# Kernel optimization log

Measured on AMD Instinct MI355X. Metric: run time of the kernel, lower is better.

Reference implementation:

```python
import jax, jax.numpy as jnp
import numpy as np

IN_F = 256
OUT_F = 512
DEG = 3
BATCH = 2048


def setup_inputs() -> dict:
    key = jax.random.key(0)
    k_x, k_p, k_q, k_w = jax.random.split(key, 4)
    x = jax.random.normal(k_x, (BATCH, IN_F), dtype=jnp.float32)
    P_coef = jax.random.normal(k_p, (OUT_F, IN_F, DEG + 1), dtype=jnp.float32) * 0.1
    Q_coef = jax.random.normal(k_q, (OUT_F, IN_F, DEG), dtype=jnp.float32) * 0.1
    # reset_parameters(): constant term of P zeroed, constant of Q set to 1
    P_coef = P_coef.at[:, :, 0].set(0.0)
    Q_coef = Q_coef.at[:, :, 0].set(1.0)
    # xavier_uniform for base_weight
    limit = float(np.sqrt(6.0 / (IN_F + OUT_F)))
    base_weight = jax.random.uniform(k_w, (OUT_F, IN_F), dtype=jnp.float32,
                                     minval=-limit, maxval=limit)
    base_bias = jnp.zeros((OUT_F,), dtype=jnp.float32)
    return {"x": x, "P_coef": P_coef, "Q_coef": Q_coef,
            "base_weight": base_weight, "base_bias": base_bias}


def reference(x, P_coef, Q_coef, base_weight, base_bias):
    # x: (B, I). Powers x^0..x^DEG -> (B, I, DEG+1)
    exps = jnp.arange(DEG + 1, dtype=x.dtype)
    x_powers = x[..., None] ** exps  # (B, I, P)
    # P[b,i,o] = sum_p P_coef[o,i,p] * x[b,i]^p
    P = jnp.einsum('oip,bip->bio', P_coef, x_powers)
    # Q uses powers x^1..x^DEG
    Q = 1.0 + jnp.einsum('oip,bip->bio', Q_coef, x_powers[:, :, 1:])
    rational = P / (Q + 1e-6)          # (B, I, O)
    rational_output = rational.sum(axis=1)  # (B, O)
    base_output = x @ base_weight.T + base_bias  # (B, O)
    return base_output + rational_output
```

## Files before the change

### kernel.cpp

```cpp
#include <hip/hip_runtime.h>

constexpr int IN_F  = 256;
constexpr int OUT_F = 512;
constexpr int BATCH = 2048;

__global__ __launch_bounds__(256) void prep_pack8_kernel(
    const float* __restrict__ p, const float* __restrict__ q,
    const float* __restrict__ w, float4* __restrict__ pk, int n) {
    int t = blockIdx.x * 256 + threadIdx.x;
    if (t < n) {
        pk[2 * t]     = make_float4(p[4 * t], p[4 * t + 1], p[4 * t + 2], p[4 * t + 3]);
        pk[2 * t + 1] = make_float4(q[3 * t], q[3 * t + 1], q[3 * t + 2], w[t]);
    }
}

template <bool PACK>
__global__ __launch_bounds__(256) void kan_kernel(
    const float*  __restrict__ x,
    const float4* __restrict__ Pc,
    const float*  __restrict__ Qc,
    const float4* __restrict__ PK,
    const float*  __restrict__ W,
    const float*  __restrict__ bias,
    float* __restrict__ out)
{
#pragma clang fp contract(off)
    const int lane = threadIdx.x & 63;
    const int wave = __builtin_amdgcn_readfirstlane(threadIdx.x >> 6);
    const int b    = blockIdx.x * 64 + lane;
    const int o0   = blockIdx.y * 8 + wave * 2;

    float acc[2] = {0.f, 0.f};
    const float* xrow = x + (size_t)b * IN_F;

    for (int ic = 0; ic < IN_F; ic += 4) {
        const float4 xq = *reinterpret_cast<const float4*>(xrow + ic);
        float x1[4] = {xq.x, xq.y, xq.z, xq.w};
        float x2[4], x3[4];
#pragma unroll
        for (int j = 0; j < 4; ++j) {
            x2[j] = x1[j] * x1[j];
            const double xd = (double)x1[j];
            x3[j] = (float)(xd * xd * xd);
        }
#pragma unroll
        for (int oo = 0; oo < 2; ++oo) {
            const int rowbase = (o0 + oo) * IN_F + ic;
#pragma unroll
            for (int j = 0; j < 4; ++j) {
                float p0, p1, p2, p3, q1, q2, q3, wv;
                if (PACK) {
                    const float4 pa = PK[2 * (rowbase + j)];
                    const float4 pb = PK[2 * (rowbase + j) + 1];
                    p0 = pa.x; p1 = pa.y; p2 = pa.z; p3 = pa.w;
                    q1 = pb.x; q2 = pb.y; q3 = pb.z; wv = pb.w;
                } else {
                    const float4 pc = Pc[rowbase + j];
                    const float* qp = Qc + (size_t)(rowbase + j) * 3;
                    p0 = pc.x; p1 = pc.y; p2 = pc.z; p3 = pc.w;
                    q1 = qp[0]; q2 = qp[1]; q3 = qp[2];
                    wv = W[rowbase + j];
                }
                float t = q1 * x1[j];
                t = fmaf(q2, x2[j], t);
                t = fmaf(q3, x3[j], t);
                float Qv = 1.0f + t;
                float Qp = Qv + 1e-6f;
                float s = fmaf(p1, x1[j], p0);
                s = fmaf(p2, x2[j], s);
                s = fmaf(p3, x3[j], s);
                const float r = __builtin_amdgcn_rcpf(Qp);
                acc[oo] = fmaf(s, r, acc[oo]);
                acc[oo] = fmaf(wv, x1[j], acc[oo]);
            }
        }
    }

    float2 res = make_float2(acc[0] + bias[o0 + 0], acc[1] + bias[o0 + 1]);
    *reinterpret_cast<float2*>(out + (size_t)b * OUT_F + o0) = res;
}

extern "C" void kernel_launch(void* const* d_in, const int* in_sizes, int n_in,
                              void* d_out, int out_size, void* d_ws, size_t ws_size,
                              hipStream_t stream) {
    const float* x    = (const float*)d_in[0];
    const float* Pc   = (const float*)d_in[1];
    const float* Qc   = (const float*)d_in[2];
    const float* W    = (const float*)d_in[3];
    const float* bias = (const float*)d_in[4];
    float* out = (float*)d_out;

    const int n = OUT_F * IN_F;
    dim3 grid(BATCH / 64, OUT_F / 8);

    if (ws_size >= (size_t)n * 32) {
        float4* pk = (float4*)d_ws;
        prep_pack8_kernel<<<(n + 255) / 256, 256, 0, stream>>>(Pc, Qc, W, pk, n);
        kan_kernel<true><<<grid, 256, 0, stream>>>(
            x, (const float4*)Pc, Qc, pk, W, bias, out);
    } else {
        kan_kernel<false><<<grid, 256, 0, stream>>>(
            x, (const float4*)Pc, Qc, nullptr, W, bias, out);
    }
}
```

Baseline: 130.1 us.

## Split input dimension across waves and reduce partial sums through LDS

Each wave now covers all 8 outputs of the block over a quarter of the input features, instead of 2 outputs over all inputs. Partial sums go to shared memory and are combined after a barrier, then written with bias. The intent is to read each x element once per block rather than once per wave and to give each thread more independent accumulators, while the launch bound now asks for higher occupancy. It adds LDS traffic, a sync, a different summation order, and register pressure from 8 accumulators under the tighter launch bound.

```diff
diff --git a/kernel.cpp b/kernel.cpp
--- a/kernel.cpp
+++ b/kernel.cpp
@@ -15,7 +15,7 @@
 }
 
 template <bool PACK>
-__global__ __launch_bounds__(256) void kan_kernel(
+__global__ __launch_bounds__(256, 8) void kan_kernel(
     const float*  __restrict__ x,
     const float4* __restrict__ Pc,
     const float*  __restrict__ Qc,
@@ -25,15 +25,16 @@
     float* __restrict__ out)
 {
 #pragma clang fp contract(off)
-    const int lane = threadIdx.x & 63;
-    const int wave = __builtin_amdgcn_readfirstlane(threadIdx.x >> 6);
-    const int b    = blockIdx.x * 64 + lane;
-    const int o0   = blockIdx.y * 8 + wave * 2;
+    const int lane  = threadIdx.x & 63;
+    const int wave  = __builtin_amdgcn_readfirstlane(threadIdx.x >> 6);
+    const int b     = blockIdx.x * 64 + lane;
+    const int o0    = blockIdx.y * 8;
+    const int ibase = wave * 64;
 
-    float acc[2] = {0.f, 0.f};
-    const float* xrow = x + (size_t)b * IN_F;
+    float acc[8] = {0.f, 0.f, 0.f, 0.f, 0.f, 0.f, 0.f, 0.f};
+    const float* xrow = x + (size_t)b * IN_F + ibase;
 
-    for (int ic = 0; ic < IN_F; ic += 4) {
+    for (int ic = 0; ic < 64; ic += 4) {
         const float4 xq = *reinterpret_cast<const float4*>(xrow + ic);
         float x1[4] = {xq.x, xq.y, xq.z, xq.w};
         float x2[4], x3[4];
@@ -43,9 +44,10 @@
             const double xd = (double)x1[j];
             x3[j] = (float)(xd * xd * xd);
         }
+        const int rowi = ibase + ic;
 #pragma unroll
-        for (int oo = 0; oo < 2; ++oo) {
-            const int rowbase = (o0 + oo) * IN_F + ic;
+        for (int oo = 0; oo < 8; ++oo) {
+            const int rowbase = (o0 + oo) * IN_F + rowi;
 #pragma unroll
             for (int j = 0; j < 4; ++j) {
                 float p0, p1, p2, p3, q1, q2, q3, wv;
@@ -76,8 +78,22 @@
         }
     }
 
-    float2 res = make_float2(acc[0] + bias[o0 + 0], acc[1] + bias[o0 + 1]);
-    *reinterpret_cast<float2*>(out + (size_t)b * OUT_F + o0) = res;
+    __shared__ float red[4 * 64 * 8];
+    float4* dst = reinterpret_cast<float4*>(&red[(wave * 64 + lane) * 8]);
+    dst[0] = make_float4(acc[0], acc[1], acc[2], acc[3]);
+    dst[1] = make_float4(acc[4], acc[5], acc[6], acc[7]);
+    __syncthreads();
+
+#pragma unroll
+    for (int k = 0; k < 2; ++k) {
+        const int idx = threadIdx.x + k * 256;
+        float s = red[idx] + red[512 + idx];
+        s = s + red[1024 + idx];
+        s = s + red[1536 + idx];
+        const int bb = idx >> 3, o = idx & 7;
+        s = s + bias[o0 + o];
+        out[(size_t)(blockIdx.x * 64 + bb) * OUT_F + o0 + o] = s;
+    }
 }
 
 extern "C" void kernel_launch(void* const* d_in, const int* in_sizes, int n_in,
```

New measurement: 107.2 us. -17.6%, faster.
